# Kernel optimization log

Measured on AMD Instinct MI355X. Metric: run time of the kernel, lower is better.

The kernel has to match this reference:

```python
import jax, jax.numpy as jnp
import numpy as np

IN_FEATURES = 4096
OUT_FEATURES = 4096
IN_GROUP = 8
OUT_GROUP = 1
NUM_CODEBOOKS = 1
CODEBOOK_SIZE = 2 ** 16
NUM_OUT_GROUPS = OUT_FEATURES // OUT_GROUP   # 4096
NUM_IN_GROUPS = IN_FEATURES // IN_GROUP      # 512


def setup_inputs() -> dict:
    key = jax.random.key(0)
    k1, k2, k3, k4, k5 = jax.random.split(key, 5)
    input = jax.random.normal(k1, (4, 2048, IN_FEATURES), dtype=jnp.float32)
    codes = jax.random.randint(k2, (NUM_OUT_GROUPS, NUM_IN_GROUPS, NUM_CODEBOOKS), 0, CODEBOOK_SIZE, dtype=jnp.int32)
    codebooks = jax.random.normal(k3, (NUM_CODEBOOKS, CODEBOOK_SIZE, OUT_GROUP, IN_GROUP), dtype=jnp.float32)
    scales = jax.random.uniform(k4, (NUM_OUT_GROUPS, 1, 1, 1), dtype=jnp.float32)
    bias = jax.random.normal(k5, (OUT_FEATURES,), dtype=jnp.float32)
    return {"input": input, "codes": codes, "codebooks": codebooks, "scales": scales, "bias": bias}


def _dequantize_weight(codes, codebooks, scales):
    # codes: [nog, nig, nc] int; codebooks: [nc, K, og, ig]; scales: [nog, 1, 1, 1]
    nc = codebooks.shape[0]
    # gather per-codebook entries: [nog, nig, nc, og, ig]
    gathered = codebooks[jnp.arange(nc), codes]
    # sum over codebooks, apply per-out-group scale -> [nog, nig, og, ig]
    w = gathered.sum(axis=2) * scales
    nog, nig, og, ig = w.shape
    # [nog, og, nig, ig] -> [out_features, in_features]
    return w.transpose(0, 2, 1, 3).reshape(nog * og, nig * ig)


def reference(input, codes, codebooks, scales, bias):
    # Faithful AQLM dequant-GEMM: reconstruct W then input @ W^T + bias
    W = _dequantize_weight(codes, codebooks, scales)  # [out, in]
    out = jnp.einsum("bso,io->bsi", input, W.T.T) if False else input @ W.T
    if bias is not None:
        out = out + bias
    return out
```

## Files before the change

kernel.cpp:

```cpp
#include <hip/hip_runtime.h>
#include <hip/hip_bf16.h>
#include <stdint.h>

#define M_DIM 8192
#define N_DIM 4096
#define K_DIM 4096
#define NOG   4096
#define NIG   512

typedef __bf16 bf16;
typedef __attribute__((ext_vector_type(8))) __bf16 bf16x8;
typedef __attribute__((ext_vector_type(4))) float f32x4;


__device__ __forceinline__ void gload16(const void* g, void* lds) {
    __builtin_amdgcn_global_load_lds(
        (__attribute__((address_space(1))) void*)g,
        (__attribute__((address_space(3))) void*)lds,
        16 , 0 , 0 );
}

__global__ __launch_bounds__(256) void k_convert_tile(const float* __restrict__ in,
                                                      bf16* __restrict__ out) {
    __shared__ __align__(16) bf16 tile[256 * 8];
    const int t   = threadIdx.x;
    const int g   = blockIdx.y;
    const int h0  = blockIdx.x * 4;
    const int row = t >> 4;
    const int cc  = t & 15;
    const float4* p = (const float4*)(in + (size_t)(g * 16 + row) * K_DIM
                                         + h0 * 32 + cc * 8);
    float4 a = p[0], b = p[1];
    bf16x8 v;
    v[0] = (bf16)a.x; v[1] = (bf16)a.y; v[2] = (bf16)a.z; v[3] = (bf16)a.w;
    v[4] = (bf16)b.x; v[5] = (bf16)b.y; v[6] = (bf16)b.z; v[7] = (bf16)b.w;
    const int widx = (cc >> 2) * 64 + (cc & 3) * 16 + row;
    ((bf16x8*)tile)[widx] = v;
    __syncthreads();
    bf16x8 o = ((bf16x8*)tile)[t];
    ((bf16x8*)out)[((size_t)g * 128 + h0) * 64 + t] = o;
}

__global__ __launch_bounds__(256) void k_dequant_tile(const int* __restrict__ codes,
                                                      const float* __restrict__ cb,
                                                      const float* __restrict__ scales,
                                                      bf16* __restrict__ w) {
    const int t    = threadIdx.x;
    const int gB   = blockIdx.y;
    const int h0   = blockIdx.x * 4;
    const int hl   = t >> 6;
    const int kblk = (t >> 4) & 3;
    const int row  = t & 15;
    const int o    = gB * 16 + row;
    const int iG   = blockIdx.x * 16 + hl * 4 + kblk;
    unsigned code = (unsigned)codes[o * NIG + iG];
    float s = scales[o];
    const float4* e = (const float4*)(cb + (size_t)code * 8);
    float4 e0 = e[0], e1 = e[1];
    bf16x8 v;
    v[0] = (bf16)(e0.x * s); v[1] = (bf16)(e0.y * s);
    v[2] = (bf16)(e0.z * s); v[3] = (bf16)(e0.w * s);
    v[4] = (bf16)(e1.x * s); v[5] = (bf16)(e1.y * s);
    v[6] = (bf16)(e1.z * s); v[7] = (bf16)(e1.w * s);
    ((bf16x8*)w)[((size_t)gB * 128 + h0) * 64 + t] = v;
}

#define BM 256
#define BN 128
#define BK 64
#define KSTEPS (K_DIM / BK)

__global__ __launch_bounds__(256, 2) void k_gemm_tiled(
    const bf16* __restrict__ A,
    const bf16* __restrict__ B,
    const float* __restrict__ bias,
    float* __restrict__ C)
{
    __shared__ __align__(16) bf16 As[BM * BK];
    __shared__ __align__(16) bf16 Bs[BN * BK];

    const int tid  = threadIdx.x;
    const int wave = tid >> 6;
    const int lane = tid & 63;
    const int quad = lane >> 4;
    const int l16  = lane & 15;

    const int bn0 = blockIdx.x * BN;
    const int bm0 = blockIdx.y * BM;
    const int wm = (wave >> 1) * 128;
    const int wn = (wave & 1) * 64;

    const bf16* pA[4];
    const bf16* pB[2];
    #pragma unroll
    for (int gi = 0; gi < 4; ++gi) {
        const int g = blockIdx.y * 16 + wave * 4 + gi;
        pA[gi] = A + ((size_t)g * 8192 + lane) * 8;
    }
    #pragma unroll
    for (int gi = 0; gi < 2; ++gi) {
        const int g = blockIdx.x * 8 + wave * 2 + gi;
        pB[gi] = B + ((size_t)g * 8192 + lane) * 8;
    }
    bf16* AsW = As + wave * 4096;
    bf16* BsW = Bs + wave * 2048;

    const int gA0 = (wave >> 1) * 8;
    const int gB0 = (wave & 1) * 4;

    f32x4 acc[8][4] = {};

    for (int ks = 0; ks < KSTEPS; ++ks) {
        #pragma unroll
        for (int gi = 0; gi < 4; ++gi) {
            gload16(pA[gi],       AsW + gi * 1024);
            gload16(pA[gi] + 512, AsW + gi * 1024 + 512);
            pA[gi] += 1024;
        }
        #pragma unroll
        for (int gi = 0; gi < 2; ++gi) {
            gload16(pB[gi],       BsW + gi * 1024);
            gload16(pB[gi] + 512, BsW + gi * 1024 + 512);
            pB[gi] += 1024;
        }
        __syncthreads();

        bf16x8 af0[8], af1[8], bq0[4], bq1[4];
        #pragma unroll
        for (int t = 0; t < 8; ++t) {
            af0[t] = *(const bf16x8*)(As + (size_t)(gA0 + t) * 1024 + lane * 8);
            af1[t] = *(const bf16x8*)(As + (size_t)(gA0 + t) * 1024 + 512 + lane * 8);
        }
        #pragma unroll
        for (int t = 0; t < 4; ++t) {
            bq0[t] = *(const bf16x8*)(Bs + (size_t)(gB0 + t) * 1024 + lane * 8);
            bq1[t] = *(const bf16x8*)(Bs + (size_t)(gB0 + t) * 1024 + 512 + lane * 8);
        }

        #pragma unroll
        for (int i = 0; i < 8; ++i)
            #pragma unroll
            for (int j = 0; j < 4; ++j)
                acc[i][j] = __builtin_amdgcn_mfma_f32_16x16x32_bf16(
                    af0[i], bq0[j], acc[i][j], 0, 0, 0);
        #pragma unroll
        for (int i = 0; i < 8; ++i)
            #pragma unroll
            for (int j = 0; j < 4; ++j)
                acc[i][j] = __builtin_amdgcn_mfma_f32_16x16x32_bf16(
                    af1[i], bq1[j], acc[i][j], 0, 0, 0);

        __syncthreads();
    }

    #pragma unroll
    for (int j = 0; j < 4; ++j) {
        const int gn = bn0 + wn + j * 16 + l16;
        const float bz = bias[gn];
        #pragma unroll
        for (int i = 0; i < 8; ++i) {
            float* cp = C + (size_t)(bm0 + wm + i * 16 + quad * 4) * N_DIM + gn;
            #pragma unroll
            for (int r = 0; r < 4; ++r)
                cp[(size_t)r * N_DIM] = acc[i][j][r] + bz;
        }
    }
}

extern "C" void kernel_launch(void* const* d_in, const int* in_sizes, int n_in,
                              void* d_out, int out_size, void* d_ws, size_t ws_size,
                              hipStream_t stream) {
    const float* input     = (const float*)d_in[0];
    const int*   codes     = (const int*)d_in[1];
    const float* codebooks = (const float*)d_in[2];
    const float* scales    = (const float*)d_in[3];
    const float* bias      = (const float*)d_in[4];
    float* out = (float*)d_out;

    bf16* Abf = (bf16*)d_ws;
    bf16* Wbf = (bf16*)((char*)d_ws + (size_t)M_DIM * K_DIM * sizeof(bf16));

    (void)in_sizes; (void)n_in; (void)out_size; (void)ws_size;

    {
        dim3 g(K_DIM / 128, M_DIM / 16);
        k_convert_tile<<<g, 256, 0, stream>>>(input, Abf);
    }
    {
        dim3 g(K_DIM / 128, NOG / 16);
        k_dequant_tile<<<g, 256, 0, stream>>>(codes, codebooks, scales, Wbf);
    }
    {
        dim3 g(N_DIM / BN, M_DIM / BM);
        k_gemm_tiled<<<g, 256, 0, stream>>>(Abf, Wbf, bias, out);
    }
}
```

Before: 460.6 us.

## Double-buffer GEMM LDS with 256x256 tiles, 8 waves and half-step pipelining

Enlarges the GEMM block tile to 256x256 and runs 512 threads (8 waves) per block. LDS is double-buffered, and each K step is split into two half phases that prefetch the next slice with direct global-to-LDS loads while MFMAs run on the current one. Hand-placed waitcnt, barriers and setprio are meant to hide global memory latency and cut synchronisation stalls. The cost is 64KB of LDS per block and higher register pressure, so fewer blocks may fit per CU, and the manual waitcnt counting is fragile.

```diff
diff --git a/kernel.cpp b/kernel.cpp
--- a/kernel.cpp
+++ b/kernel.cpp
@@ -66,18 +66,56 @@
 }
 
 #define BM 256
-#define BN 128
+#define BN 256
 #define BK 64
 #define KSTEPS (K_DIM / BK)
 
-__global__ __launch_bounds__(256, 2) void k_gemm_tiled(
+__device__ __forceinline__ void gemm_phase(
+    const bf16* __restrict__ AsR, const bf16* __restrict__ BsR,
+    bf16* __restrict__ AsW, bf16* __restrict__ BsW,
+    const bf16* paw0, const bf16* paw1, const bf16* pbw0, const bf16* pbw1,
+    int gA0, int gB0, int lane, const int h, int ss,
+    f32x4 (&acc)[8][4])
+{
+    bf16x8 af[8], bq[4];
+    #pragma unroll
+    for (int m = 0; m < 8; ++m)
+        af[m] = *(const bf16x8*)(AsR + (size_t)(gA0 + m) * 1024 + h * 512 + lane * 8);
+    #pragma unroll
+    for (int j = 0; j < 4; ++j)
+        bq[j] = *(const bf16x8*)(BsR + (size_t)(gB0 + j) * 1024 + h * 512 + lane * 8);
+
+    if (ss < 128) {
+        gload16(paw0 + (size_t)ss * 512, AsW + h * 512);
+        gload16(paw1 + (size_t)ss * 512, AsW + 1024 + h * 512);
+        gload16(pbw0 + (size_t)ss * 512, BsW + h * 512);
+        gload16(pbw1 + (size_t)ss * 512, BsW + 1024 + h * 512);
+    }
+
+    asm volatile("s_waitcnt vmcnt(4)" ::: "memory");
+    __builtin_amdgcn_s_barrier();
+    asm volatile("s_waitcnt lgkmcnt(0)" ::: "memory");
+    __builtin_amdgcn_sched_barrier(0);
+
+    __builtin_amdgcn_s_setprio(1);
+    #pragma unroll
+    for (int i = 0; i < 8; ++i)
+        #pragma unroll
+        for (int j = 0; j < 4; ++j)
+            acc[i][j] = __builtin_amdgcn_mfma_f32_16x16x32_bf16(
+                af[i], bq[j], acc[i][j], 0, 0, 0);
+    __builtin_amdgcn_s_setprio(0);
+    __builtin_amdgcn_s_barrier();
+}
+
+__global__ __launch_bounds__(512, 2) void k_gemm_tiled(
     const bf16* __restrict__ A,
     const bf16* __restrict__ B,
     const float* __restrict__ bias,
     float* __restrict__ C)
 {
-    __shared__ __align__(16) bf16 As[BM * BK];
-    __shared__ __align__(16) bf16 Bs[BN * BK];
+    __shared__ __align__(16) bf16 As[2][16 * 1024];
+    __shared__ __align__(16) bf16 Bs[2][16 * 1024];
 
     const int tid  = threadIdx.x;
     const int wave = tid >> 6;
@@ -87,70 +125,43 @@
 
     const int bn0 = blockIdx.x * BN;
     const int bm0 = blockIdx.y * BM;
-    const int wm = (wave >> 1) * 128;
-    const int wn = (wave & 1) * 64;
-
-    const bf16* pA[4];
-    const bf16* pB[2];
-    #pragma unroll
-    for (int gi = 0; gi < 4; ++gi) {
-        const int g = blockIdx.y * 16 + wave * 4 + gi;
-        pA[gi] = A + ((size_t)g * 8192 + lane) * 8;
-    }
-    #pragma unroll
-    for (int gi = 0; gi < 2; ++gi) {
-        const int g = blockIdx.x * 8 + wave * 2 + gi;
-        pB[gi] = B + ((size_t)g * 8192 + lane) * 8;
-    }
-    bf16* AsW = As + wave * 4096;
-    bf16* BsW = Bs + wave * 2048;
-
-    const int gA0 = (wave >> 1) * 8;
-    const int gB0 = (wave & 1) * 4;
+    const int wm  = (wave >> 2) * 128;
+    const int wn  = (wave & 3) * 64;
+    const int gA0 = (wave >> 2) * 8;
+    const int gB0 = (wave & 3) * 4;
+
+    const bf16* paw0 = A + ((size_t)(blockIdx.y * 16 + wave * 2 + 0) * 8192 + lane) * 8;
+    const bf16* paw1 = A + ((size_t)(blockIdx.y * 16 + wave * 2 + 1) * 8192 + lane) * 8;
+    const bf16* pbw0 = B + ((size_t)(blockIdx.x * 16 + wave * 2 + 0) * 8192 + lane) * 8;
+    const bf16* pbw1 = B + ((size_t)(blockIdx.x * 16 + wave * 2 + 1) * 8192 + lane) * 8;
+
+    bf16* As0w = &As[0][wave * 2048];
+    bf16* As1w = &As[1][wave * 2048];
+    bf16* Bs0w = &Bs[0][wave * 2048];
+    bf16* Bs1w = &Bs[1][wave * 2048];
+
+    gload16(paw0,       As0w);        gload16(paw1,       As0w + 1024);
+    gload16(pbw0,       Bs0w);        gload16(pbw1,       Bs0w + 1024);
+    gload16(paw0 + 512, As0w + 512);  gload16(paw1 + 512, As0w + 1536);
+    gload16(pbw0 + 512, Bs0w + 512);  gload16(pbw1 + 512, Bs0w + 1536);
+    asm volatile("s_waitcnt vmcnt(4)" ::: "memory");
+    __builtin_amdgcn_s_barrier();
 
     f32x4 acc[8][4] = {};
 
-    for (int ks = 0; ks < KSTEPS; ++ks) {
-        #pragma unroll
-        for (int gi = 0; gi < 4; ++gi) {
-            gload16(pA[gi],       AsW + gi * 1024);
-            gload16(pA[gi] + 512, AsW + gi * 1024 + 512);
-            pA[gi] += 1024;
-        }
-        #pragma unroll
-        for (int gi = 0; gi < 2; ++gi) {
-            gload16(pB[gi],       BsW + gi * 1024);
-            gload16(pB[gi] + 512, BsW + gi * 1024 + 512);
-            pB[gi] += 1024;
-        }
-        __syncthreads();
-
-        bf16x8 af0[8], af1[8], bq0[4], bq1[4];
-        #pragma unroll
-        for (int t = 0; t < 8; ++t) {
-            af0[t] = *(const bf16x8*)(As + (size_t)(gA0 + t) * 1024 + lane * 8);
-            af1[t] = *(const bf16x8*)(As + (size_t)(gA0 + t) * 1024 + 512 + lane * 8);
-        }
-        #pragma unroll
-        for (int t = 0; t < 4; ++t) {
-            bq0[t] = *(const bf16x8*)(Bs + (size_t)(gB0 + t) * 1024 + lane * 8);
-            bq1[t] = *(const bf16x8*)(Bs + (size_t)(gB0 + t) * 1024 + 512 + lane * 8);
-        }
-
-        #pragma unroll
-        for (int i = 0; i < 8; ++i)
-            #pragma unroll
-            for (int j = 0; j < 4; ++j)
-                acc[i][j] = __builtin_amdgcn_mfma_f32_16x16x32_bf16(
-                    af0[i], bq0[j], acc[i][j], 0, 0, 0);
-        #pragma unroll
-        for (int i = 0; i < 8; ++i)
-            #pragma unroll
-            for (int j = 0; j < 4; ++j)
-                acc[i][j] = __builtin_amdgcn_mfma_f32_16x16x32_bf16(
-                    af1[i], bq1[j], acc[i][j], 0, 0, 0);
-
-        __syncthreads();
+    const bf16* AsR0 = &As[0][0]; const bf16* BsR0 = &Bs[0][0];
+    const bf16* AsR1 = &As[1][0]; const bf16* BsR1 = &Bs[1][0];
+
+    for (int ks = 0; ks < KSTEPS; ks += 2) {
+        const int s0 = ks * 2;
+        gemm_phase(AsR0, BsR0, As1w, Bs1w, paw0, paw1, pbw0, pbw1,
+                   gA0, gB0, lane, 0, s0 + 2, acc);
+        gemm_phase(AsR0, BsR0, As1w, Bs1w, paw0, paw1, pbw0, pbw1,
+                   gA0, gB0, lane, 1, s0 + 3, acc);
+        gemm_phase(AsR1, BsR1, As0w, Bs0w, paw0, paw1, pbw0, pbw1,
+                   gA0, gB0, lane, 0, s0 + 4, acc);
+        gemm_phase(AsR1, BsR1, As0w, Bs0w, paw0, paw1, pbw0, pbw1,
+                   gA0, gB0, lane, 1, s0 + 5, acc);
     }
 
     #pragma unroll
@@ -192,6 +203,6 @@
     }
     {
         dim3 g(N_DIM / BN, M_DIM / BM);
-        k_gemm_tiled<<<g, 256, 0, stream>>>(Abf, Wbf, bias, out);
-    }
-}
+        k_gemm_tiled<<<g, 512, 0, stream>>>(Abf, Wbf, bias, out);
+    }
+}
```

Result: no change. 457.5 us (-0.7%).
